# Performance work log

Measured on AMD Instinct MI355X. Metric: run time of the kernel, lower is better.

## Reference

```python
import jax, jax.numpy as jnp
import numpy as np
import math


def _l2norm(x, axis):
    n = jnp.sqrt(jnp.sum(x * x, axis=axis, keepdims=True))
    return x / jnp.maximum(n, 1e-12)


def _look_back(x):
    # circular shift of buckets by one along dim1, concat along window dim2
    shift = jnp.concatenate([x[:, -1:], x[:, :-1]], axis=1)
    return jnp.concatenate([shift, x], axis=2)


def _get_dup_keys(x, rounds):
    # x: [B, L, K] int; counts duplicates of each key within its row
    idx = jnp.argsort(x, axis=-1)
    s = jnp.take_along_axis(x, idx, axis=-1)
    cnt = jnp.ones(x.shape, dtype=jnp.int32)
    for i in range(1, rounds):
        eq = (s[..., i:] == s[..., :-i]).astype(jnp.int32)
        cnt = cnt.at[..., i:].add(eq)
        cnt = cnt.at[..., :-i].add(eq)
    inv = jnp.argsort(idx, axis=-1)  # unsort
    return jnp.take_along_axis(cnt, inv, axis=-1)


def _forward(query, value, rand_matrix):
    B, L, dk = query.shape
    R = rand_matrix.shape[2]
    nb = 2 * rand_matrix.shape[3]          # n_buckets
    bl = L // nb                            # bucket_length

    # ---- LSH hashing ----
    rm = rand_matrix / jnp.linalg.norm(rand_matrix, axis=1, keepdims=True)
    q_n = _l2norm(query, -1)
    mm = jnp.einsum('bld,bdrn->blrn', q_n, rm)            # [B,L,R,nb/2]
    hashes = jnp.argmax(jnp.concatenate([mm, -mm], axis=-1), axis=-1).astype(jnp.int32)
    hashes = hashes * L + jnp.arange(L, dtype=jnp.int32)[None, :, None]  # [B,L,R]

    hash_indice = jnp.argsort(hashes, axis=1)             # sort positions per round
    sorted_hashes = jnp.take_along_axis(hashes, hash_indice, axis=1)
    original_indice = jnp.argsort(hash_indice, axis=1)    # inverse permutation

    def gather_bld(x, idx):  # x [B,L,dk], idx [B,L,R] -> [B,L,dk,R]
        xe = jnp.broadcast_to(x[..., None], (B, L, dk, R))
        ie = jnp.broadcast_to(idx[:, :, None, :], (B, L, dk, R))
        return jnp.take_along_axis(xe, ie, axis=1)

    rq = gather_bld(query, hash_indice).reshape(B, nb, bl, dk, R)
    lk = _l2norm(_look_back(rq), axis=-2)                 # [B,nb,2bl,dk,R]
    mqk = jnp.einsum('bnidr,bnjdr->bnijr', rq, lk) / math.sqrt(dk)  # [B,nb,bl,2bl,R]

    # bucket mismatch mask, then causal masks (order matters: == overwrites)
    sh = (sorted_hashes // L).reshape(B, nb, bl, R)
    mqk = jnp.where(sh[:, :, :, None, :] != _look_back(sh)[:, :, None, :, :], -1e9, mqk)
    qi = hash_indice.reshape(B, nb, bl, R).astype(jnp.int32)
    ki = _look_back(qi)                                    # [B,nb,2bl,R]
    mqk = jnp.where(qi[:, :, :, None, :] < ki[:, :, None, :, :], -1e9, mqk)
    mqk = jnp.where(qi[:, :, :, None, :] == ki[:, :, None, :, :], -1e5, mqk)

    # duplicate-key counts (computed in original order, regathered to sorted order)
    ki_full = jnp.broadcast_to(ki[:, :, None, :, :], (B, nb, bl, 2 * bl, R)).reshape(B, L, 2 * bl, R)
    oi = jnp.broadcast_to(original_indice[:, :, None, :], (B, L, 2 * bl, R))
    ki_orig = jnp.take_along_axis(ki_full, oi, axis=1)
    count_key = _get_dup_keys(ki_orig.reshape(B, L, 2 * bl * R), R).reshape(B, L, 2 * bl, R)
    hi = jnp.broadcast_to(hash_indice[:, :, None, :], (B, L, 2 * bl, R))
    count_key = jnp.take_along_axis(count_key, hi, axis=1)

    mqk_flat = mqk.reshape(B, L, 2 * bl, R)
    lse = jax.scipy.special.logsumexp(mqk_flat, axis=2)   # [B,L,R]
    sm = jnp.exp(mqk_flat - jnp.log(count_key.astype(mqk.dtype)) - lse[:, :, None, :])

    rv = gather_bld(value, hash_indice).reshape(B, nb, bl, dk, R)
    att = jnp.einsum('bnijr,bnjdr->bnidr', sm.reshape(B, nb, bl, 2 * bl, R), _look_back(rv))
    att = att.reshape(B, L, dk, R)
    di = jnp.broadcast_to(original_indice[:, :, None, :], (B, L, dk, R))
    att = jnp.take_along_axis(att, di, axis=1)             # back to original order

    lse_o = jnp.take_along_axis(lse, original_indice, axis=1)
    w = jax.nn.softmax(lse_o, axis=1)                      # faithful: dim=1 as in source
    return jnp.einsum('bldr,blr->bld', att, w)


def setup_inputs() -> dict:
    key = jax.random.key(0)
    k1, k2, k3 = jax.random.split(key, 3)
    B, L, DK, R, BL = 16, 4096, 64, 4, 64
    NB = L // BL
    query = jax.random.normal(k1, (B, L, DK), dtype=jnp.float32)
    value = jax.random.normal(k2, (B, L, DK), dtype=jnp.float32)
    rand_matrix = jax.random.normal(k3, (B, DK, R, NB // 2), dtype=jnp.float32)
    return {"query": query, "value": value, "rand_matrix": rand_matrix, "seed": 0}


def reference(query, value, rand_matrix, seed):
    # eval mode: deterministic_dropout is skipped; seed unused
    return _forward(query, value, rand_matrix)
```

## Files before the change

### kernel.cpp

```cpp
#include <hip/hip_runtime.h>

#define B_ 16
#define L_ 4096
#define DK_ 64
#define R_ 4
#define NB_ 64
#define BL_ 64

typedef __attribute__((ext_vector_type(8))) short bf16x8;
typedef __attribute__((ext_vector_type(4))) float f32x4;

__device__ __forceinline__ float bf2f(unsigned short u) {
  return __uint_as_float(((unsigned)u) << 16);
}
__device__ __forceinline__ unsigned cvtpk(float lo, float hi) {
  unsigned r;
  asm("v_cvt_pk_bf16_f32 %0, %1, %2" : "=v"(r) : "v"(lo), "v"(hi));
  return r;
}
__device__ __forceinline__ int swz(int row) { return (row & 7) ^ ((row >> 3) & 7); }

__global__ __launch_bounds__(128) void prep_kernel(
    const float* __restrict__ rm, double* __restrict__ sinvd) {
  int b = blockIdx.x;
  int t = threadIdx.x;
  const float* rb = rm + (size_t)b * (DK_ * 128);
  double ss = 0.0;
  for (int d = 0; d < DK_; ++d) {
    double v = (double)rb[d * 128 + t];
    ss += v * v;
  }
  sinvd[b * 128 + t] = 1.0 / sqrt(ss);
}

__global__ __launch_bounds__(256) void hash_kernel(
    const float* __restrict__ query, const float* __restrict__ rm,
    const double* __restrict__ sinvd, int* __restrict__ bucket) {
  __shared__ float qs[64 * 68];
  __shared__ float rs[64 * 136];
  __shared__ double ssin[128];
  __shared__ int sb[64 * 4];

  int b = blockIdx.x >> 6;
  int tok0 = (blockIdx.x & 63) << 6;
  int t = threadIdx.x;

  {
    const float4* qg = (const float4*)(query + ((size_t)b * L_ + tok0) * DK_);
    #pragma unroll
    for (int u = 0; u < 4; ++u) {
      int i = t + u * 256;
      int tokl = i >> 4, c4 = i & 15;
      *(float4*)(qs + tokl * 68 + c4 * 4) = qg[i];
    }
  }
  {
    const float4* rg = (const float4*)(rm + (size_t)b * (DK_ * 128));
    #pragma unroll
    for (int u = 0; u < 8; ++u) {
      int i = t + u * 256;
      int d = i >> 5, c4 = i & 31;
      *(float4*)(rs + d * 136 + c4 * 4) = rg[i];
    }
  }
  if (t < 128) ssin[t] = sinvd[b * 128 + t];
  __syncthreads();

  int cg = t & 7;
  int tg = t >> 3;
  double acc0[16], acc1[16];
  #pragma unroll
  for (int j = 0; j < 16; ++j) { acc0[j] = 0.0; acc1[j] = 0.0; }

  const float* q0 = qs + (tg * 2 + 0) * 68;
  const float* q1 = qs + (tg * 2 + 1) * 68;
  const float* rp = rs + cg * 16;
  for (int d = 0; d < DK_; ++d) {
    double qa = (double)q0[d];
    double qb = (double)q1[d];
    const float* rr = rp + d * 136;
    #pragma unroll
    for (int j4 = 0; j4 < 4; ++j4) {
      float4 rv = *(const float4*)(rr + j4 * 4);
      double r0 = (double)rv.x, r1 = (double)rv.y,
             r2 = (double)rv.z, r3 = (double)rv.w;
      acc0[j4 * 4 + 0] += qa * r0; acc0[j4 * 4 + 1] += qa * r1;
      acc0[j4 * 4 + 2] += qa * r2; acc0[j4 * 4 + 3] += qa * r3;
      acc1[j4 * 4 + 0] += qb * r0; acc1[j4 * 4 + 1] += qb * r1;
      acc1[j4 * 4 + 2] += qb * r2; acc1[j4 * 4 + 3] += qb * r3;
    }
  }

  double bv0 = -1e300, bv1 = -1e300;
  int bi0 = 0, bi1 = 0;
  int nbase = (cg & 1) * 16;
  #pragma unroll
  for (int j = 0; j < 16; ++j) {
    int col = cg * 16 + j;
    double sv = ssin[col];
    int n = nbase + j;
    double v0 = acc0[j] * sv;
    double v1 = acc1[j] * sv;
    if (v0 > bv0 || (v0 == bv0 && n < bi0)) { bv0 = v0; bi0 = n; }
    if (-v0 > bv0 || (-v0 == bv0 && n + 32 < bi0)) { bv0 = -v0; bi0 = n + 32; }
    if (v1 > bv1 || (v1 == bv1 && n < bi1)) { bv1 = v1; bi1 = n; }
    if (-v1 > bv1 || (-v1 == bv1 && n + 32 < bi1)) { bv1 = -v1; bi1 = n + 32; }
  }
  {
    double ov = __shfl_xor(bv0, 1);
    int oi = __shfl_xor(bi0, 1);
    if (ov > bv0 || (ov == bv0 && oi < bi0)) { bv0 = ov; bi0 = oi; }
    ov = __shfl_xor(bv1, 1);
    oi = __shfl_xor(bi1, 1);
    if (ov > bv1 || (ov == bv1 && oi < bi1)) { bv1 = ov; bi1 = oi; }
  }
  if ((cg & 1) == 0) {
    int rr_ = cg >> 1;
    sb[(tg * 2 + 0) * 4 + rr_] = bi0;
    sb[(tg * 2 + 1) * 4 + rr_] = bi1;
  }
  __syncthreads();
  if (t < 64)
    ((int4*)bucket)[(size_t)b * L_ + tok0 + t] = ((int4*)sb)[t];
}

__global__ __launch_bounds__(1024) void sort_kernel(
    const int* __restrict__ bucket, int* __restrict__ sorted_pos,
    unsigned char* __restrict__ cpack) {
  int b = blockIdx.x >> 2;
  int r = blockIdx.x & 3;
  __shared__ int hist[64 * 65];
  __shared__ int off[64];
  int t = threadIdx.x, lane = t & 63, w = t >> 6;
  unsigned long long ltmask = (1ull << lane) - 1ull;
  const int* bb = bucket + (size_t)b * L_ * 4 + r;

  int binv[4], rank[4];
  #pragma unroll
  for (int u = 0; u < 4; ++u)
    binv[u] = bb[(size_t)((w * 4 + u) * 64 + lane) * 4];

  for (int idx = t; idx < 64 * 65; idx += 1024) hist[idx] = 0;
  __syncthreads();

  #pragma unroll
  for (int u = 0; u < 4; ++u) {
    int bin = binv[u];
    unsigned long long m = ~0ull;
    #pragma unroll
    for (int k = 0; k < 6; ++k) {
      unsigned long long bal = __ballot((bin >> k) & 1);
      m &= ((bin >> k) & 1) ? bal : ~bal;
    }
    rank[u] = (int)__popcll(m & ltmask);
    if (rank[u] == 0) hist[(w * 4 + u) * 65 + bin] = (int)__popcll(m);
  }
  __syncthreads();

  if (w == 0) {
    int run = 0;
    for (int g = 0; g < 64; ++g) {
      int v = hist[g * 65 + lane];
      hist[g * 65 + lane] = run;
      run += v;
    }
    int inc = run;
    #pragma unroll
    for (int d = 1; d < 64; d <<= 1) {
      int y = __shfl_up(inc, d, 64);
      if (lane >= d) inc += y;
    }
    off[lane] = inc - run;
  }
  __syncthreads();

  int* sp = sorted_pos + ((size_t)b * R_ + r) * L_;
  unsigned char* cp = cpack + (size_t)b * L_ * 4 + r;
  #pragma unroll
  for (int u = 0; u < 4; ++u) {
    int g = w * 4 + u;
    int bin = binv[u];
    int slot = off[bin] + hist[g * 65 + bin] + rank[u];
    sp[slot] = g * 64 + lane;
    cp[(size_t)(g * 64 + lane) * 4] = (unsigned char)(slot >> 6);
  }
}

__global__ __launch_bounds__(256) void attn_kernel(
    const float* __restrict__ query, const float* __restrict__ value,
    const int* __restrict__ sorted_pos, const int* __restrict__ bucket,
    const int* __restrict__ cpack,
    unsigned short* __restrict__ att, float* __restrict__ lse_s) {
  int wg = (int)blockIdx.x;
  wg = (wg & 7) * (B_ * R_ * NB_ / 8) + (wg >> 3);
  int n = wg & 63;
  int r = (wg >> 6) & 3;
  int b = wg >> 8;

  __shared__ __align__(16) short bufK[128 * 64];
  __shared__ float ssca[64];
  __shared__ int skpos[128];
  __shared__ int skcode[128];
  __shared__ int sck[128];

  int t = threadIdx.x;
  const int* sp = sorted_pos + ((size_t)b * R_ + r) * L_;

  if (t < 128) {
    int chunk = (t < 64) ? ((n + 63) & 63) : n;
    int pos = sp[chunk * 64 + (t & 63)];
    int bkt = bucket[((size_t)b * L_ + pos) * 4 + r];
    skpos[t] = pos;
    skcode[t] = (bkt << 12) | pos;
    sck[t] = ((const int*)cpack)[(size_t)b * L_ + pos];
  }
  __syncthreads();

  {
    int j = t >> 1, half = t & 1;
    const float* qr = query + ((size_t)b * L_ + skpos[j]) * DK_ + half * 32;
    float v[32];
    float ss = 0.f;
    #pragma unroll
    for (int u = 0; u < 8; ++u) {
      float4 x = ((const float4*)qr)[u];
      v[u*4+0] = x.x; v[u*4+1] = x.y; v[u*4+2] = x.z; v[u*4+3] = x.w;
      ss += x.x*x.x + x.y*x.y + x.z*x.z + x.w*x.w;
    }
    ss += __shfl_xor(ss, 1);
    float inv = 1.0f / fmaxf(sqrtf(ss), 1e-12f);
    short* krow = bufK + j * 64;
    #pragma unroll
    for (int u = 0; u < 4; ++u) {
      int d0 = half * 32 + u * 8;
      uint4 pk;
      pk.x = cvtpk(v[u*8+0] * inv, v[u*8+1] * inv);
      pk.y = cvtpk(v[u*8+2] * inv, v[u*8+3] * inv);
      pk.z = cvtpk(v[u*8+4] * inv, v[u*8+5] * inv);
      pk.w = cvtpk(v[u*8+6] * inv, v[u*8+7] * inv);
      *(uint4*)(krow + (((d0 >> 3) ^ swz(j)) << 3)) = pk;
    }
    if (j >= 64 && half == 0) ssca[j - 64] = 0.18033688f / inv;
  }
  __syncthreads();

  int l = t & 63, w = t >> 6;
  int g = l >> 4, c = l & 15;
  f32x4 acc[8];
  #pragma unroll
  for (int tt = 0; tt < 8; ++tt) acc[tt] = (f32x4){0.f, 0.f, 0.f, 0.f};
  {
    int qrow = 64 + w * 16 + c;
    const short* qp_ = bufK + qrow * 64;
    bf16x8 q0 = *(const bf16x8*)(qp_ + (((g) ^ swz(qrow)) << 3));
    bf16x8 q1 = *(const bf16x8*)(qp_ + (((4 + g) ^ swz(qrow)) << 3));
    #pragma unroll
    for (int tt = 0; tt < 8; ++tt) {
      int krow = tt * 16 + c;
      const short* kp_ = bufK + krow * 64;
      bf16x8 k0 = *(const bf16x8*)(kp_ + (((g) ^ swz(krow)) << 3));
      bf16x8 k1 = *(const bf16x8*)(kp_ + (((4 + g) ^ swz(krow)) << 3));
      acc[tt] = __builtin_amdgcn_mfma_f32_16x16x32_bf16(k0, q0, acc[tt], 0, 0, 0);
      acc[tt] = __builtin_amdgcn_mfma_f32_16x16x32_bf16(k1, q1, acc[tt], 0, 0, 0);
    }
  }
  __syncthreads();

  int pi = t >> 2, qd = t & 3;
  const float* vr0 = value + ((size_t)b * L_ + skpos[2 * pi]) * DK_ + qd * 16;
  const float* vr1 = value + ((size_t)b * L_ + skpos[2 * pi + 1]) * DK_ + qd * 16;
  float4 va[4], vb4[4];
  #pragma unroll
  for (int c4 = 0; c4 < 4; ++c4) { va[c4] = ((const float4*)vr0)[c4]; vb4[c4] = ((const float4*)vr1)[c4]; }

  int qi = w * 16 + c;
  int qcode = skcode[64 + qi];
  unsigned aq = (unsigned)sck[64 + qi] | 0x40404040u;
  float csc = ssca[qi];
  int qpos = qcode & 4095;

  float m = -1e30f;
  #pragma unroll
  for (int tt = 0; tt < 8; ++tt) {
    int4 kc = *(const int4*)(skcode + tt * 16 + g * 4);
    #pragma unroll
    for (int j = 0; j < 4; ++j) {
      int kcode = (j == 0) ? kc.x : (j == 1) ? kc.y : (j == 2) ? kc.z : kc.w;
      float s = acc[tt][j] * csc;
      unsigned x = (unsigned)(qcode ^ kcode);
      s = ((qcode < kcode) || (x >= 4096u)) ? -1e9f : s;
      s = (x == 0u) ? -144269.5f : s;
      acc[tt][j] = s;
      m = fmaxf(m, s);
    }
  }
  m = fmaxf(m, __shfl_xor(m, 16));
  m = fmaxf(m, __shfl_xor(m, 32));
  float sum = 0.f;
  #pragma unroll
  for (int tt = 0; tt < 8; ++tt) {
    #pragma unroll
    for (int j = 0; j < 4; ++j) {
      float e = exp2f(acc[tt][j] - m);
      acc[tt][j] = e;
      sum += e;
    }
  }
  sum += __shfl_xor(sum, 16);
  sum += __shfl_xor(sum, 32);
  float lse = 0.69314718f * (m + __log2f(sum));
  float isum = 1.0f / sum;
  if (l < 16) lse_s[((size_t)b * R_ + r) * L_ + qpos] = lse;

  #pragma unroll
  for (int tt = 0; tt < 8; ++tt) {
    int4 c4v = *(const int4*)(sck + tt * 16 + g * 4);
    #pragma unroll
    for (int j = 0; j < 4; ++j) {
      int ckv = (j == 0) ? c4v.x : (j == 1) ? c4v.y : (j == 2) ? c4v.z : c4v.w;
      unsigned e = (aq - (unsigned)ckv) & 0x3E3E3E3Eu;
      unsigned y = (e - 0x01010101u) & ~e & 0x80808080u;
      float cntf = (float)__popc(y);
      acc[tt][j] = acc[tt][j] * isum * __builtin_amdgcn_rcpf(cntf);
    }
  }

  unsigned pk01[8], pk23[8];
  #pragma unroll
  for (int tt = 0; tt < 8; ++tt) {
    pk01[tt] = cvtpk(acc[tt][0], acc[tt][1]);
    pk23[tt] = cvtpk(acc[tt][2], acc[tt][3]);
  }

  short* VT = bufK;
  #pragma unroll
  for (int c4 = 0; c4 < 4; ++c4) {
    float4 x0 = va[c4], x1 = vb4[c4];
    #pragma unroll
    for (int cc = 0; cc < 4; ++cc) {
      float f0 = (cc == 0) ? x0.x : (cc == 1) ? x0.y : (cc == 2) ? x0.z : x0.w;
      float f1 = (cc == 0) ? x1.x : (cc == 1) ? x1.y : (cc == 2) ? x1.z : x1.w;
      unsigned pk2 = cvtpk(f0, f1);
      int nrow = qd * 16 + c4 * 4 + cc;
      int k0 = 2 * pi;
      int a = nrow * 128 + (((k0 >> 3) ^ swz(nrow)) << 3) + (k0 & 7);
      *(unsigned*)(VT + a) = pk2;
    }
  }
  __syncthreads();

  f32x4 o[4];
  #pragma unroll
  for (int nt = 0; nt < 4; ++nt) o[nt] = (f32x4){0.f, 0.f, 0.f, 0.f};
  {
    int src  = (g & 1) * 32 + c;
    int srcB = src + 16;
    bool sel = (l >= 32);
    #pragma unroll
    for (int ks = 0; ks < 4; ++ks) {
      unsigned xA = __shfl(pk01[2 * ks], src),  yA = __shfl(pk01[2 * ks + 1], src);
      unsigned xB = __shfl(pk23[2 * ks], src),  yB = __shfl(pk23[2 * ks + 1], src);
      unsigned xC = __shfl(pk01[2 * ks], srcB), yC = __shfl(pk01[2 * ks + 1], srcB);
      unsigned xD = __shfl(pk23[2 * ks], srcB), yD = __shfl(pk23[2 * ks + 1], srcB);
      union { uint4 u; bf16x8 v; } bp;
      bp.u.x = sel ? yA : xA;
      bp.u.y = sel ? yB : xB;
      bp.u.z = sel ? yC : xC;
      bp.u.w = sel ? yD : xD;
      #pragma unroll
      for (int nt = 0; nt < 4; ++nt) {
        int vrow = nt * 16 + c;
        bf16x8 av = *(const bf16x8*)(VT + vrow * 128 + (((ks * 4 + g) ^ swz(vrow)) << 3));
        o[nt] = __builtin_amdgcn_mfma_f32_16x16x32_bf16(av, bp.v, o[nt], 0, 0, 0);
      }
    }
  }

  {
    unsigned short* arow = att + (((size_t)b * R_ + r) * L_ + qpos) * DK_;
    #pragma unroll
    for (int nt = 0; nt < 4; ++nt) {
      unsigned p0 = cvtpk(o[nt][0], o[nt][1]);
      unsigned p1 = cvtpk(o[nt][2], o[nt][3]);
      *(uint2*)(arow + nt * 16 + g * 4) = make_uint2(p0, p1);
    }
  }
}

__global__ __launch_bounds__(256) void lsered_kernel(
    const float* __restrict__ lse_s, float* __restrict__ wred) {
  int br = blockIdx.x;
  const float* row = lse_s + (size_t)br * L_;
  __shared__ float red[4];
  int t = threadIdx.x;
  float m = -1e30f;
  for (int p = t; p < L_; p += 256) m = fmaxf(m, row[p]);
  #pragma unroll
  for (int mask = 1; mask < 64; mask <<= 1) m = fmaxf(m, __shfl_xor(m, mask, 64));
  if ((t & 63) == 0) red[t >> 6] = m;
  __syncthreads();
  m = fmaxf(fmaxf(red[0], red[1]), fmaxf(red[2], red[3]));
  __syncthreads();
  float sum = 0.f;
  for (int p = t; p < L_; p += 256) sum += __expf(row[p] - m);
  #pragma unroll
  for (int mask = 1; mask < 64; mask <<= 1) sum += __shfl_xor(sum, mask, 64);
  if ((t & 63) == 0) red[t >> 6] = sum;
  __syncthreads();
  if (t == 0) {
    wred[br * 2] = m;
    wred[br * 2 + 1] = red[0] + red[1] + red[2] + red[3];
  }
}

__global__ __launch_bounds__(256) void combine_kernel(
    const unsigned short* __restrict__ att, const float* __restrict__ lse_s,
    const float* __restrict__ wred, float* __restrict__ out) {
  int idx = blockIdx.x * 256 + threadIdx.x;
  int dq = idx & 3;
  int l = (idx >> 2) & (L_ - 1);
  int b = idx >> 14;
  float wv[4];
  #pragma unroll
  for (int r = 0; r < R_; ++r) {
    float m = wred[(b * R_ + r) * 2];
    float sinv = 1.0f / wred[(b * R_ + r) * 2 + 1];
    wv[r] = __expf(lse_s[((size_t)b * R_ + r) * L_ + l] - m) * sinv;
  }
  #pragma unroll
  for (int u = 0; u < 4; ++u) {
    int d4 = dq * 4 + u;
    float4 o = make_float4(0.f, 0.f, 0.f, 0.f);
    #pragma unroll
    for (int r = 0; r < R_; ++r) {
      ushort4 a = *(const ushort4*)(att + ((((size_t)b * R_ + r) * L_ + l) * 16 + d4) * 4);
      o.x += wv[r] * bf2f(a.x); o.y += wv[r] * bf2f(a.y);
      o.z += wv[r] * bf2f(a.z); o.w += wv[r] * bf2f(a.w);
    }
    ((float4*)out)[((size_t)b * L_ + l) * 16 + d4] = o;
  }
}

extern "C" void kernel_launch(void* const* d_in, const int* in_sizes, int n_in,
                              void* d_out, int out_size, void* d_ws, size_t ws_size,
                              hipStream_t stream) {
  const float* query = (const float*)d_in[0];
  const float* value = (const float*)d_in[1];
  const float* rm    = (const float*)d_in[2];
  (void)in_sizes; (void)n_in; (void)out_size; (void)ws_size;

  char* ws = (char*)d_ws;
  const size_t ATT_BYTES = (size_t)B_ * R_ * L_ * DK_ * 2;
  const size_t MB = 1048576;
  unsigned short* att        = (unsigned short*)ws;
  int*            bucket     = (int*)(ws + ATT_BYTES);
  int*            sorted_pos = (int*)(ws + ATT_BYTES + 1 * MB);
  unsigned char*  cpack      = (unsigned char*)(ws + ATT_BYTES + 2 * MB);
  float*          lse_s      = (float*)(ws + ATT_BYTES + 3 * MB);
  float*          wred       = (float*)(ws + ATT_BYTES + 4 * MB);
  double*         sinvd      = (double*)(ws + ATT_BYTES + 5 * MB);
  float* out = (float*)d_out;

  prep_kernel<<<B_, 128, 0, stream>>>(rm, sinvd);
  hash_kernel<<<B_ * 64, 256, 0, stream>>>(query, rm, sinvd, bucket);
  sort_kernel<<<B_ * R_, 1024, 0, stream>>>(bucket, sorted_pos, cpack);
  attn_kernel<<<B_ * R_ * NB_, 256, 0, stream>>>(query, value, sorted_pos, bucket,
                                                 (const int*)cpack, att, lse_s);
  lsered_kernel<<<B_ * R_, 256, 0, stream>>>(lse_s, wred);
  combine_kernel<<<(B_ * L_ * 4) / 256, 256, 0, stream>>>(att, lse_s, wred, out);
}
```

Before: 120.8 us.

## Precompute normalized bf16 K and transposed V per chunk in separate kernel

Adds a kvprep kernel that gathers query and value rows in sorted order once per chunk. It writes normalized bf16 K tiles, pre-transposed bf16 V tiles in swizzled layout, and per-row scales to workspace. The attention kernel then loads these tiles straight into LDS and stages P through LDS instead of using cross-lane shuffles. Previously each chunk was gathered and normalized twice, once as the current chunk and once as the look-back chunk, with scattered fp32 loads. The cost is an extra kernel launch and a write-then-read round trip of about 64 MB of bf16 workspace.

```diff
diff --git a/kernel.cpp b/kernel.cpp
--- a/kernel.cpp
+++ b/kernel.cpp
@@ -186,8 +186,69 @@
   }
 }
 
+__global__ __launch_bounds__(256) void kvprep_kernel(
+    const float* __restrict__ query, const float* __restrict__ value,
+    const int* __restrict__ sorted_pos,
+    unsigned short* __restrict__ Kng, unsigned short* __restrict__ VTg,
+    float* __restrict__ sscal) {
+  int wg = (int)blockIdx.x;
+  int chunk = wg & 63, r = (wg >> 6) & 3, b = wg >> 8;
+  int br = b * R_ + r;
+  __shared__ float vs[64 * 65];
+  __shared__ int spos[64];
+  int t = threadIdx.x;
+  if (t < 64) spos[t] = sorted_pos[(size_t)br * L_ + chunk * 64 + t];
+  __syncthreads();
+  int row = t >> 2, qd = t & 3;
+  int pos = spos[row];
+
+  const float* qr = query + ((size_t)b * L_ + pos) * DK_ + qd * 16;
+  float4 x0 = ((const float4*)qr)[0], x1 = ((const float4*)qr)[1],
+         x2 = ((const float4*)qr)[2], x3 = ((const float4*)qr)[3];
+  float ss = x0.x*x0.x + x0.y*x0.y + x0.z*x0.z + x0.w*x0.w
+           + x1.x*x1.x + x1.y*x1.y + x1.z*x1.z + x1.w*x1.w
+           + x2.x*x2.x + x2.y*x2.y + x2.z*x2.z + x2.w*x2.w
+           + x3.x*x3.x + x3.y*x3.y + x3.z*x3.z + x3.w*x3.w;
+  ss += __shfl_xor(ss, 1);
+  ss += __shfl_xor(ss, 2);
+  float inv = 1.0f / fmaxf(sqrtf(ss), 1e-12f);
+  uint4 pk0, pk1;
+  pk0.x = cvtpk(x0.x*inv, x0.y*inv); pk0.y = cvtpk(x0.z*inv, x0.w*inv);
+  pk0.z = cvtpk(x1.x*inv, x1.y*inv); pk0.w = cvtpk(x1.z*inv, x1.w*inv);
+  pk1.x = cvtpk(x2.x*inv, x2.y*inv); pk1.y = cvtpk(x2.z*inv, x2.w*inv);
+  pk1.z = cvtpk(x3.x*inv, x3.y*inv); pk1.w = cvtpk(x3.z*inv, x3.w*inv);
+  unsigned short* kr = Kng + (((size_t)br * 64 + chunk) * 64 + row) * 64;
+  *(uint4*)(kr + (((qd * 2    ) ^ swz(row)) << 3)) = pk0;
+  *(uint4*)(kr + (((qd * 2 + 1) ^ swz(row)) << 3)) = pk1;
+  if (qd == 0) sscal[(size_t)br * L_ + chunk * 64 + row] = 0.18033688f / inv;
+
+  const float* vr = value + ((size_t)b * L_ + pos) * DK_ + qd * 16;
+  float4 v0 = ((const float4*)vr)[0], v1 = ((const float4*)vr)[1],
+         v2 = ((const float4*)vr)[2], v3 = ((const float4*)vr)[3];
+  float* vw = vs + row * 65 + qd * 16;
+  vw[0]=v0.x; vw[1]=v0.y; vw[2]=v0.z; vw[3]=v0.w;
+  vw[4]=v1.x; vw[5]=v1.y; vw[6]=v1.z; vw[7]=v1.w;
+  vw[8]=v2.x; vw[9]=v2.y; vw[10]=v2.z; vw[11]=v2.w;
+  vw[12]=v3.x; vw[13]=v3.y; vw[14]=v3.z; vw[15]=v3.w;
+  __syncthreads();
+
+  int d = t >> 2, kg = t & 3;
+  float vv[16];
+  #pragma unroll
+  for (int kk = 0; kk < 16; ++kk) vv[kk] = vs[(kg * 16 + kk) * 65 + d];
+  uint4 a0, a1;
+  a0.x = cvtpk(vv[0], vv[1]);  a0.y = cvtpk(vv[2], vv[3]);
+  a0.z = cvtpk(vv[4], vv[5]);  a0.w = cvtpk(vv[6], vv[7]);
+  a1.x = cvtpk(vv[8], vv[9]);  a1.y = cvtpk(vv[10], vv[11]);
+  a1.z = cvtpk(vv[12], vv[13]); a1.w = cvtpk(vv[14], vv[15]);
+  unsigned short* vt = VTg + (((size_t)br * 64 + chunk) * 64 + d) * 64;
+  *(uint4*)(vt + (((kg * 2    ) ^ swz(d)) << 3)) = a0;
+  *(uint4*)(vt + (((kg * 2 + 1) ^ swz(d)) << 3)) = a1;
+}
+
 __global__ __launch_bounds__(256) void attn_kernel(
-    const float* __restrict__ query, const float* __restrict__ value,
+    const unsigned short* __restrict__ Kng, const unsigned short* __restrict__ VTg,
+    const float* __restrict__ sscal,
     const int* __restrict__ sorted_pos, const int* __restrict__ bucket,
     const int* __restrict__ cpack,
     unsigned short* __restrict__ att, float* __restrict__ lse_s) {
@@ -196,68 +257,60 @@
   int n = wg & 63;
   int r = (wg >> 6) & 3;
   int b = wg >> 8;
-
-  __shared__ __align__(16) short bufK[128 * 64];
-  __shared__ float ssca[64];
-  __shared__ int skpos[128];
+  int br = b * R_ + r;
+  int nprev = (n + 63) & 63;
+
+  __shared__ __align__(16) uint4 stage[2048];
+  short* ldsK  = (short*)stage;
+  short* ldsVT = (short*)(stage + 1024);
+  short* ldsP  = (short*)stage;
   __shared__ int skcode[128];
   __shared__ int sck[128];
 
   int t = threadIdx.x;
-  const int* sp = sorted_pos + ((size_t)b * R_ + r) * L_;
-
-  if (t < 128) {
-    int chunk = (t < 64) ? ((n + 63) & 63) : n;
-    int pos = sp[chunk * 64 + (t & 63)];
-    int bkt = bucket[((size_t)b * L_ + pos) * 4 + r];
-    skpos[t] = pos;
-    skcode[t] = (bkt << 12) | pos;
-    sck[t] = ((const int*)cpack)[(size_t)b * L_ + pos];
-  }
-  __syncthreads();
-
-  {
-    int j = t >> 1, half = t & 1;
-    const float* qr = query + ((size_t)b * L_ + skpos[j]) * DK_ + half * 32;
-    float v[32];
-    float ss = 0.f;
-    #pragma unroll
-    for (int u = 0; u < 8; ++u) {
-      float4 x = ((const float4*)qr)[u];
-      v[u*4+0] = x.x; v[u*4+1] = x.y; v[u*4+2] = x.z; v[u*4+3] = x.w;
-      ss += x.x*x.x + x.y*x.y + x.z*x.z + x.w*x.w;
-    }
-    ss += __shfl_xor(ss, 1);
-    float inv = 1.0f / fmaxf(sqrtf(ss), 1e-12f);
-    short* krow = bufK + j * 64;
-    #pragma unroll
-    for (int u = 0; u < 4; ++u) {
-      int d0 = half * 32 + u * 8;
-      uint4 pk;
-      pk.x = cvtpk(v[u*8+0] * inv, v[u*8+1] * inv);
-      pk.y = cvtpk(v[u*8+2] * inv, v[u*8+3] * inv);
-      pk.z = cvtpk(v[u*8+4] * inv, v[u*8+5] * inv);
-      pk.w = cvtpk(v[u*8+6] * inv, v[u*8+7] * inv);
-      *(uint4*)(krow + (((d0 >> 3) ^ swz(j)) << 3)) = pk;
-    }
-    if (j >= 64 && half == 0) ssca[j - 64] = 0.18033688f / inv;
-  }
-  __syncthreads();
-
   int l = t & 63, w = t >> 6;
   int g = l >> 4, c = l & 15;
+  int qi = w * 16 + c;
+
+  if (t < 128) {
+    int chunk = (t < 64) ? nprev : n;
+    int pos = sorted_pos[(size_t)br * L_ + chunk * 64 + (t & 63)];
+    skcode[t] = (bucket[((size_t)b * L_ + pos) * 4 + r] << 12) | pos;
+    sck[t] = ((const int*)cpack)[(size_t)b * L_ + pos];
+  }
+
+  {
+    const uint4* ksrc0 = (const uint4*)(Kng + ((size_t)br * 64 + nprev) * 64 * 64);
+    const uint4* ksrc1 = (const uint4*)(Kng + ((size_t)br * 64 + n) * 64 * 64);
+    #pragma unroll
+    for (int u = 0; u < 2; ++u) stage[u * 256 + t] = ksrc0[u * 256 + t];
+    #pragma unroll
+    for (int u = 0; u < 2; ++u) stage[512 + u * 256 + t] = ksrc1[u * 256 + t];
+    const uint4* vt0 = (const uint4*)(VTg + ((size_t)br * 64 + nprev) * 64 * 64);
+    const uint4* vt1 = (const uint4*)(VTg + ((size_t)br * 64 + n) * 64 * 64);
+    #pragma unroll
+    for (int u = 0; u < 4; ++u) {
+      int unit = u * 256 + t;
+      int vrow = unit >> 4, s16 = unit & 15;
+      const uint4* src = (s16 >> 3) ? vt1 : vt0;
+      stage[1024 + unit] = src[vrow * 8 + (s16 & 7)];
+    }
+  }
+  float csc = sscal[(size_t)br * L_ + n * 64 + qi];
+  __syncthreads();
+
   f32x4 acc[8];
   #pragma unroll
   for (int tt = 0; tt < 8; ++tt) acc[tt] = (f32x4){0.f, 0.f, 0.f, 0.f};
   {
-    int qrow = 64 + w * 16 + c;
-    const short* qp_ = bufK + qrow * 64;
+    int qrow = 64 + qi;
+    const short* qp_ = ldsK + qrow * 64;
     bf16x8 q0 = *(const bf16x8*)(qp_ + (((g) ^ swz(qrow)) << 3));
     bf16x8 q1 = *(const bf16x8*)(qp_ + (((4 + g) ^ swz(qrow)) << 3));
     #pragma unroll
     for (int tt = 0; tt < 8; ++tt) {
       int krow = tt * 16 + c;
-      const short* kp_ = bufK + krow * 64;
+      const short* kp_ = ldsK + krow * 64;
       bf16x8 k0 = *(const bf16x8*)(kp_ + (((g) ^ swz(krow)) << 3));
       bf16x8 k1 = *(const bf16x8*)(kp_ + (((4 + g) ^ swz(krow)) << 3));
       acc[tt] = __builtin_amdgcn_mfma_f32_16x16x32_bf16(k0, q0, acc[tt], 0, 0, 0);
@@ -266,17 +319,8 @@
   }
   __syncthreads();
 
-  int pi = t >> 2, qd = t & 3;
-  const float* vr0 = value + ((size_t)b * L_ + skpos[2 * pi]) * DK_ + qd * 16;
-  const float* vr1 = value + ((size_t)b * L_ + skpos[2 * pi + 1]) * DK_ + qd * 16;
-  float4 va[4], vb4[4];
-  #pragma unroll
-  for (int c4 = 0; c4 < 4; ++c4) { va[c4] = ((const float4*)vr0)[c4]; vb4[c4] = ((const float4*)vr1)[c4]; }
-
-  int qi = w * 16 + c;
   int qcode = skcode[64 + qi];
   unsigned aq = (unsigned)sck[64 + qi] | 0x40404040u;
-  float csc = ssca[qi];
   int qpos = qcode & 4095;
 
   float m = -1e30f;
@@ -310,7 +354,7 @@
   sum += __shfl_xor(sum, 32);
   float lse = 0.69314718f * (m + __log2f(sum));
   float isum = 1.0f / sum;
-  if (l < 16) lse_s[((size_t)b * R_ + r) * L_ + qpos] = lse;
+  if (l < 16) lse_s[(size_t)br * L_ + qpos] = lse;
 
   #pragma unroll
   for (int tt = 0; tt < 8; ++tt) {
@@ -324,27 +368,14 @@
       acc[tt][j] = acc[tt][j] * isum * __builtin_amdgcn_rcpf(cntf);
     }
   }
-
-  unsigned pk01[8], pk23[8];
-  #pragma unroll
-  for (int tt = 0; tt < 8; ++tt) {
-    pk01[tt] = cvtpk(acc[tt][0], acc[tt][1]);
-    pk23[tt] = cvtpk(acc[tt][2], acc[tt][3]);
-  }
-
-  short* VT = bufK;
-  #pragma unroll
-  for (int c4 = 0; c4 < 4; ++c4) {
-    float4 x0 = va[c4], x1 = vb4[c4];
-    #pragma unroll
-    for (int cc = 0; cc < 4; ++cc) {
-      float f0 = (cc == 0) ? x0.x : (cc == 1) ? x0.y : (cc == 2) ? x0.z : x0.w;
-      float f1 = (cc == 0) ? x1.x : (cc == 1) ? x1.y : (cc == 2) ? x1.z : x1.w;
-      unsigned pk2 = cvtpk(f0, f1);
-      int nrow = qd * 16 + c4 * 4 + cc;
-      int k0 = 2 * pi;
-      int a = nrow * 128 + (((k0 >> 3) ^ swz(nrow)) << 3) + (k0 & 7);
-      *(unsigned*)(VT + a) = pk2;
+  {
+    #pragma unroll
+    for (int tt = 0; tt < 8; ++tt) {
+      unsigned p01 = cvtpk(acc[tt][0], acc[tt][1]);
+      unsigned p23 = cvtpk(acc[tt][2], acc[tt][3]);
+      int slot = tt * 2 + (g >> 1);
+      int off = qi * 128 + ((slot ^ swz(qi)) << 3) + (g & 1) * 4;
+      *(uint2*)(ldsP + off) = make_uint2(p01, p23);
     }
   }
   __syncthreads();
@@ -353,31 +384,21 @@
   #pragma unroll
   for (int nt = 0; nt < 4; ++nt) o[nt] = (f32x4){0.f, 0.f, 0.f, 0.f};
   {
-    int src  = (g & 1) * 32 + c;
-    int srcB = src + 16;
-    bool sel = (l >= 32);
+    int prow = w * 16 + c;
     #pragma unroll
     for (int ks = 0; ks < 4; ++ks) {
-      unsigned xA = __shfl(pk01[2 * ks], src),  yA = __shfl(pk01[2 * ks + 1], src);
-      unsigned xB = __shfl(pk23[2 * ks], src),  yB = __shfl(pk23[2 * ks + 1], src);
-      unsigned xC = __shfl(pk01[2 * ks], srcB), yC = __shfl(pk01[2 * ks + 1], srcB);
-      unsigned xD = __shfl(pk23[2 * ks], srcB), yD = __shfl(pk23[2 * ks + 1], srcB);
-      union { uint4 u; bf16x8 v; } bp;
-      bp.u.x = sel ? yA : xA;
-      bp.u.y = sel ? yB : xB;
-      bp.u.z = sel ? yC : xC;
-      bp.u.w = sel ? yD : xD;
+      bf16x8 bp = *(const bf16x8*)(ldsP + prow * 128 + ((((ks * 4 + g)) ^ swz(prow)) << 3));
       #pragma unroll
       for (int nt = 0; nt < 4; ++nt) {
         int vrow = nt * 16 + c;
-        bf16x8 av = *(const bf16x8*)(VT + vrow * 128 + (((ks * 4 + g) ^ swz(vrow)) << 3));
-        o[nt] = __builtin_amdgcn_mfma_f32_16x16x32_bf16(av, bp.v, o[nt], 0, 0, 0);
+        bf16x8 av = *(const bf16x8*)(ldsVT + vrow * 128 + (((ks * 4 + g) ^ swz(vrow)) << 3));
+        o[nt] = __builtin_amdgcn_mfma_f32_16x16x32_bf16(av, bp, o[nt], 0, 0, 0);
       }
     }
   }
 
   {
-    unsigned short* arow = att + (((size_t)b * R_ + r) * L_ + qpos) * DK_;
+    unsigned short* arow = att + ((size_t)br * L_ + qpos) * DK_;
     #pragma unroll
     for (int nt = 0; nt < 4; ++nt) {
       unsigned p0 = cvtpk(o[nt][0], o[nt][1]);
@@ -459,13 +480,19 @@
   float*          lse_s      = (float*)(ws + ATT_BYTES + 3 * MB);
   float*          wred       = (float*)(ws + ATT_BYTES + 4 * MB);
   double*         sinvd      = (double*)(ws + ATT_BYTES + 5 * MB);
+  float*          sscal      = (float*)(ws + ATT_BYTES + 6 * MB);
+  unsigned short* Kng        = (unsigned short*)(ws + ATT_BYTES + 8 * MB);
+  unsigned short* VTg        = (unsigned short*)(ws + ATT_BYTES + 40 * MB);
   float* out = (float*)d_out;
 
   prep_kernel<<<B_, 128, 0, stream>>>(rm, sinvd);
   hash_kernel<<<B_ * 64, 256, 0, stream>>>(query, rm, sinvd, bucket);
   sort_kernel<<<B_ * R_, 1024, 0, stream>>>(bucket, sorted_pos, cpack);
-  attn_kernel<<<B_ * R_ * NB_, 256, 0, stream>>>(query, value, sorted_pos, bucket,
-                                                 (const int*)cpack, att, lse_s);
+  kvprep_kernel<<<B_ * R_ * NB_, 256, 0, stream>>>(query, value, sorted_pos,
+                                                   Kng, VTg, sscal);
+  attn_kernel<<<B_ * R_ * NB_, 256, 0, stream>>>(Kng, VTg, sscal, sorted_pos,
+                                                 bucket, (const int*)cpack,
+                                                 att, lse_s);
   lsered_kernel<<<B_ * R_, 256, 0, stream>>>(lse_s, wred);
   combine_kernel<<<(B_ * L_ * 4) / 256, 256, 0, stream>>>(att, lse_s, wred, out);
 }
```

New measurement: 134.7 us. 1.12x slower.

## Precompute normalized bf16 queries and bf16 values once before attention gather

Applied to the files above, without the earlier changes.

The hash kernel now also L2-normalizes each query row, stores it as bf16 together with its scale factor, and a new kernel converts value to bf16 once. The attention kernel then gathers bf16 rows instead of fp32 rows, which halves gather traffic and avoids redoing normalization and conversion for every round and the look-back duplicate. The rs shared-memory layout in the hash kernel is also padded differently, and query reads there are vectorized. In exchange there is an extra kernel launch and extra workspace writes and reads.

```diff
diff --git a/kernel.cpp b/kernel.cpp
--- a/kernel.cpp
+++ b/kernel.cpp
@@ -35,9 +35,10 @@
 
 __global__ __launch_bounds__(256) void hash_kernel(
     const float* __restrict__ query, const float* __restrict__ rm,
-    const double* __restrict__ sinvd, int* __restrict__ bucket) {
+    const double* __restrict__ sinvd, int* __restrict__ bucket,
+    unsigned short* __restrict__ Qn, float* __restrict__ qscale) {
   __shared__ float qs[64 * 68];
-  __shared__ float rs[64 * 136];
+  __shared__ float rs[64 * 160];
   __shared__ double ssin[128];
   __shared__ int sb[64 * 4];
 
@@ -60,7 +61,8 @@
     for (int u = 0; u < 8; ++u) {
       int i = t + u * 256;
       int d = i >> 5, c4 = i & 31;
-      *(float4*)(rs + d * 136 + c4 * 4) = rg[i];
+      int cg2 = c4 >> 2, j4 = c4 & 3;
+      *(float4*)(rs + d * 160 + cg2 * 20 + j4 * 4) = rg[i];
     }
   }
   if (t < 128) ssin[t] = sinvd[b * 128 + t];
@@ -74,20 +76,25 @@
 
   const float* q0 = qs + (tg * 2 + 0) * 68;
   const float* q1 = qs + (tg * 2 + 1) * 68;
-  const float* rp = rs + cg * 16;
-  for (int d = 0; d < DK_; ++d) {
-    double qa = (double)q0[d];
-    double qb = (double)q1[d];
-    const float* rr = rp + d * 136;
-    #pragma unroll
-    for (int j4 = 0; j4 < 4; ++j4) {
-      float4 rv = *(const float4*)(rr + j4 * 4);
-      double r0 = (double)rv.x, r1 = (double)rv.y,
-             r2 = (double)rv.z, r3 = (double)rv.w;
-      acc0[j4 * 4 + 0] += qa * r0; acc0[j4 * 4 + 1] += qa * r1;
-      acc0[j4 * 4 + 2] += qa * r2; acc0[j4 * 4 + 3] += qa * r3;
-      acc1[j4 * 4 + 0] += qb * r0; acc1[j4 * 4 + 1] += qb * r1;
-      acc1[j4 * 4 + 2] += qb * r2; acc1[j4 * 4 + 3] += qb * r3;
+  const float* rp = rs + cg * 20;
+  for (int d4 = 0; d4 < 16; ++d4) {
+    float4 qa4 = *(const float4*)(q0 + d4 * 4);
+    float4 qb4 = *(const float4*)(q1 + d4 * 4);
+    #pragma unroll
+    for (int sub = 0; sub < 4; ++sub) {
+      double qa = (double)((sub == 0) ? qa4.x : (sub == 1) ? qa4.y : (sub == 2) ? qa4.z : qa4.w);
+      double qb = (double)((sub == 0) ? qb4.x : (sub == 1) ? qb4.y : (sub == 2) ? qb4.z : qb4.w);
+      const float* rr = rp + (d4 * 4 + sub) * 160;
+      #pragma unroll
+      for (int j4 = 0; j4 < 4; ++j4) {
+        float4 rv = *(const float4*)(rr + j4 * 4);
+        double r0 = (double)rv.x, r1 = (double)rv.y,
+               r2 = (double)rv.z, r3 = (double)rv.w;
+        acc0[j4 * 4 + 0] += qa * r0; acc0[j4 * 4 + 1] += qa * r1;
+        acc0[j4 * 4 + 2] += qa * r2; acc0[j4 * 4 + 3] += qa * r3;
+        acc1[j4 * 4 + 0] += qb * r0; acc1[j4 * 4 + 1] += qb * r1;
+        acc1[j4 * 4 + 2] += qb * r2; acc1[j4 * 4 + 3] += qb * r3;
+      }
     }
   }
 
@@ -122,6 +129,33 @@
   __syncthreads();
   if (t < 64)
     ((int4*)bucket)[(size_t)b * L_ + tok0 + t] = ((int4*)sb)[t];
+
+  if (t < 128) {
+    int row = t >> 1, half = t & 1;
+    const float* qp = qs + row * 68 + half * 32;
+    float v[32];
+    float ss = 0.f;
+    #pragma unroll
+    for (int u = 0; u < 8; ++u) {
+      float4 x = *(const float4*)(qp + u * 4);
+      v[u*4+0] = x.x; v[u*4+1] = x.y; v[u*4+2] = x.z; v[u*4+3] = x.w;
+      ss += x.x*x.x + x.y*x.y + x.z*x.z + x.w*x.w;
+    }
+    ss += __shfl_xor(ss, 1);
+    float inv = 1.0f / fmaxf(sqrtf(ss), 1e-12f);
+    unsigned short* qn = Qn + ((size_t)b * L_ + tok0 + row) * 64 + half * 32;
+    #pragma unroll
+    for (int u = 0; u < 4; ++u) {
+      uint4 pk;
+      pk.x = cvtpk(v[u*8+0] * inv, v[u*8+1] * inv);
+      pk.y = cvtpk(v[u*8+2] * inv, v[u*8+3] * inv);
+      pk.z = cvtpk(v[u*8+4] * inv, v[u*8+5] * inv);
+      pk.w = cvtpk(v[u*8+6] * inv, v[u*8+7] * inv);
+      ((uint4*)qn)[u] = pk;
+    }
+    if (half == 0)
+      qscale[(size_t)b * L_ + tok0 + row] = 0.18033688f / inv;
+  }
 }
 
 __global__ __launch_bounds__(1024) void sort_kernel(
@@ -186,8 +220,31 @@
   }
 }
 
+__global__ __launch_bounds__(256) void vconv_kernel(
+    const float* __restrict__ value, unsigned short* __restrict__ Vb) {
+  int h = blockIdx.x * 256 + threadIdx.x;
+  const float* vr = value + (size_t)h * 32;
+  float v[32];
+  #pragma unroll
+  for (int u = 0; u < 8; ++u) {
+    float4 x = ((const float4*)vr)[u];
+    v[u*4+0] = x.x; v[u*4+1] = x.y; v[u*4+2] = x.z; v[u*4+3] = x.w;
+  }
+  unsigned short* out = Vb + (size_t)h * 32;
+  #pragma unroll
+  for (int u = 0; u < 4; ++u) {
+    uint4 pk;
+    pk.x = cvtpk(v[u*8+0], v[u*8+1]);
+    pk.y = cvtpk(v[u*8+2], v[u*8+3]);
+    pk.z = cvtpk(v[u*8+4], v[u*8+5]);
+    pk.w = cvtpk(v[u*8+6], v[u*8+7]);
+    ((uint4*)out)[u] = pk;
+  }
+}
+
 __global__ __launch_bounds__(256) void attn_kernel(
-    const float* __restrict__ query, const float* __restrict__ value,
+    const unsigned short* __restrict__ Qn, const unsigned short* __restrict__ Vb,
+    const float* __restrict__ qscale,
     const int* __restrict__ sorted_pos, const int* __restrict__ bucket,
     const int* __restrict__ cpack,
     unsigned short* __restrict__ att, float* __restrict__ lse_s) {
@@ -196,61 +253,47 @@
   int n = wg & 63;
   int r = (wg >> 6) & 3;
   int b = wg >> 8;
+  int br = b * R_ + r;
+  int nprev = (n + 63) & 63;
 
   __shared__ __align__(16) short bufK[128 * 64];
-  __shared__ float ssca[64];
   __shared__ int skpos[128];
   __shared__ int skcode[128];
   __shared__ int sck[128];
 
   int t = threadIdx.x;
-  const int* sp = sorted_pos + ((size_t)b * R_ + r) * L_;
-
   if (t < 128) {
-    int chunk = (t < 64) ? ((n + 63) & 63) : n;
-    int pos = sp[chunk * 64 + (t & 63)];
-    int bkt = bucket[((size_t)b * L_ + pos) * 4 + r];
+    int chunk = (t < 64) ? nprev : n;
+    int pos = sorted_pos[(size_t)br * L_ + chunk * 64 + (t & 63)];
     skpos[t] = pos;
-    skcode[t] = (bkt << 12) | pos;
+    skcode[t] = (bucket[((size_t)b * L_ + pos) * 4 + r] << 12) | pos;
     sck[t] = ((const int*)cpack)[(size_t)b * L_ + pos];
-  }
-  __syncthreads();
-
-  {
-    int j = t >> 1, half = t & 1;
-    const float* qr = query + ((size_t)b * L_ + skpos[j]) * DK_ + half * 32;
-    float v[32];
-    float ss = 0.f;
-    #pragma unroll
-    for (int u = 0; u < 8; ++u) {
-      float4 x = ((const float4*)qr)[u];
-      v[u*4+0] = x.x; v[u*4+1] = x.y; v[u*4+2] = x.z; v[u*4+3] = x.w;
-      ss += x.x*x.x + x.y*x.y + x.z*x.z + x.w*x.w;
-    }
-    ss += __shfl_xor(ss, 1);
-    float inv = 1.0f / fmaxf(sqrtf(ss), 1e-12f);
-    short* krow = bufK + j * 64;
-    #pragma unroll
-    for (int u = 0; u < 4; ++u) {
-      int d0 = half * 32 + u * 8;
-      uint4 pk;
-      pk.x = cvtpk(v[u*8+0] * inv, v[u*8+1] * inv);
-      pk.y = cvtpk(v[u*8+2] * inv, v[u*8+3] * inv);
-      pk.z = cvtpk(v[u*8+4] * inv, v[u*8+5] * inv);
-      pk.w = cvtpk(v[u*8+6] * inv, v[u*8+7] * inv);
-      *(uint4*)(krow + (((d0 >> 3) ^ swz(j)) << 3)) = pk;
-    }
-    if (j >= 64 && half == 0) ssca[j - 64] = 0.18033688f / inv;
   }
   __syncthreads();
 
   int l = t & 63, w = t >> 6;
   int g = l >> 4, c = l & 15;
+  int qi = w * 16 + c;
+
+  {
+    int j = t >> 1, half = t & 1;
+    const uint4* src = (const uint4*)(Qn + ((size_t)b * L_ + skpos[j]) * 64 + half * 32);
+    short* krow = bufK + j * 64;
+    int sz = swz(j);
+    #pragma unroll
+    for (int u = 0; u < 4; ++u)
+      *(uint4*)(krow + (((half * 4 + u) ^ sz) << 3)) = src[u];
+  }
+  int qcode = skcode[64 + qi];
+  int qpos = qcode & 4095;
+  float csc = qscale[(size_t)b * L_ + qpos];
+  __syncthreads();
+
   f32x4 acc[8];
   #pragma unroll
   for (int tt = 0; tt < 8; ++tt) acc[tt] = (f32x4){0.f, 0.f, 0.f, 0.f};
   {
-    int qrow = 64 + w * 16 + c;
+    int qrow = 64 + qi;
     const short* qp_ = bufK + qrow * 64;
     bf16x8 q0 = *(const bf16x8*)(qp_ + (((g) ^ swz(qrow)) << 3));
     bf16x8 q1 = *(const bf16x8*)(qp_ + (((4 + g) ^ swz(qrow)) << 3));
@@ -267,17 +310,12 @@
   __syncthreads();
 
   int pi = t >> 2, qd = t & 3;
-  const float* vr0 = value + ((size_t)b * L_ + skpos[2 * pi]) * DK_ + qd * 16;
-  const float* vr1 = value + ((size_t)b * L_ + skpos[2 * pi + 1]) * DK_ + qd * 16;
-  float4 va[4], vb4[4];
-  #pragma unroll
-  for (int c4 = 0; c4 < 4; ++c4) { va[c4] = ((const float4*)vr0)[c4]; vb4[c4] = ((const float4*)vr1)[c4]; }
-
-  int qi = w * 16 + c;
-  int qcode = skcode[64 + qi];
+  const uint4* vr0 = (const uint4*)(Vb + ((size_t)b * L_ + skpos[2 * pi]) * 64 + qd * 16);
+  const uint4* vr1 = (const uint4*)(Vb + ((size_t)b * L_ + skpos[2 * pi + 1]) * 64 + qd * 16);
+  uint4 A0 = vr0[0], A1 = vr0[1];
+  uint4 B0 = vr1[0], B1 = vr1[1];
+
   unsigned aq = (unsigned)sck[64 + qi] | 0x40404040u;
-  float csc = ssca[qi];
-  int qpos = qcode & 4095;
 
   float m = -1e30f;
   #pragma unroll
@@ -310,7 +348,7 @@
   sum += __shfl_xor(sum, 32);
   float lse = 0.69314718f * (m + __log2f(sum));
   float isum = 1.0f / sum;
-  if (l < 16) lse_s[((size_t)b * R_ + r) * L_ + qpos] = lse;
+  if (l < 16) lse_s[(size_t)br * L_ + qpos] = lse;
 
   #pragma unroll
   for (int tt = 0; tt < 8; ++tt) {
@@ -333,18 +371,17 @@
   }
 
   short* VT = bufK;
-  #pragma unroll
-  for (int c4 = 0; c4 < 4; ++c4) {
-    float4 x0 = va[c4], x1 = vb4[c4];
-    #pragma unroll
-    for (int cc = 0; cc < 4; ++cc) {
-      float f0 = (cc == 0) ? x0.x : (cc == 1) ? x0.y : (cc == 2) ? x0.z : x0.w;
-      float f1 = (cc == 0) ? x1.x : (cc == 1) ? x1.y : (cc == 2) ? x1.z : x1.w;
-      unsigned pk2 = cvtpk(f0, f1);
-      int nrow = qd * 16 + c4 * 4 + cc;
-      int k0 = 2 * pi;
-      int a = nrow * 128 + (((k0 >> 3) ^ swz(nrow)) << 3) + (k0 & 7);
-      *(unsigned*)(VT + a) = pk2;
+  {
+    unsigned Aw[8] = {A0.x, A0.y, A0.z, A0.w, A1.x, A1.y, A1.z, A1.w};
+    unsigned Bw[8] = {B0.x, B0.y, B0.z, B0.w, B1.x, B1.y, B1.z, B1.w};
+    int k0 = 2 * pi;
+    #pragma unroll
+    for (int i = 0; i < 8; ++i) {
+      unsigned lo = (Aw[i] & 0xffffu) | (Bw[i] << 16);
+      unsigned hi = (Aw[i] >> 16) | (Bw[i] & 0xffff0000u);
+      int dl = qd * 16 + 2 * i, dh = dl + 1;
+      *(unsigned*)(VT + dl * 128 + (((k0 >> 3) ^ swz(dl)) << 3) + (k0 & 7)) = lo;
+      *(unsigned*)(VT + dh * 128 + (((k0 >> 3) ^ swz(dh)) << 3) + (k0 & 7)) = hi;
     }
   }
   __syncthreads();
@@ -377,7 +414,7 @@
   }
 
   {
-    unsigned short* arow = att + (((size_t)b * R_ + r) * L_ + qpos) * DK_;
+    unsigned short* arow = att + ((size_t)br * L_ + qpos) * DK_;
     #pragma unroll
     for (int nt = 0; nt < 4; ++nt) {
       unsigned p0 = cvtpk(o[nt][0], o[nt][1]);
@@ -459,13 +496,18 @@
   float*          lse_s      = (float*)(ws + ATT_BYTES + 3 * MB);
   float*          wred       = (float*)(ws + ATT_BYTES + 4 * MB);
   double*         sinvd      = (double*)(ws + ATT_BYTES + 5 * MB);
+  float*          qscale     = (float*)(ws + ATT_BYTES + 6 * MB);
+  unsigned short* Qn         = (unsigned short*)(ws + ATT_BYTES + 8 * MB);
+  unsigned short* Vb         = (unsigned short*)(ws + ATT_BYTES + 16 * MB);
   float* out = (float*)d_out;
 
   prep_kernel<<<B_, 128, 0, stream>>>(rm, sinvd);
-  hash_kernel<<<B_ * 64, 256, 0, stream>>>(query, rm, sinvd, bucket);
+  hash_kernel<<<B_ * 64, 256, 0, stream>>>(query, rm, sinvd, bucket, Qn, qscale);
   sort_kernel<<<B_ * R_, 1024, 0, stream>>>(bucket, sorted_pos, cpack);
-  attn_kernel<<<B_ * R_ * NB_, 256, 0, stream>>>(query, value, sorted_pos, bucket,
-                                                 (const int*)cpack, att, lse_s);
+  vconv_kernel<<<(B_ * L_ * 2) / 256, 256, 0, stream>>>(value, Vb);
+  attn_kernel<<<B_ * R_ * NB_, 256, 0, stream>>>(Qn, Vb, qscale, sorted_pos,
+                                                 bucket, (const int*)cpack,
+                                                 att, lse_s);
   lsered_kernel<<<B_ * R_, 256, 0, stream>>>(lse_s, wred);
   combine_kernel<<<(B_ * L_ * 4) / 256, 256, 0, stream>>>(att, lse_s, wred, out);
 }
```

New measurement: 114.2 us. 5.5% less time.
